# Kernel tuning notes

Measured on AMD Instinct MI355X. Metric: run time of the kernel, lower is better.

## Reference

```python
import jax, jax.numpy as jnp
import numpy as np

B, S, D, F, E = 4, 2048, 1024, 4096, 8
LN_EPS = 1e-5


def setup_inputs() -> dict:
    key = jax.random.key(0)
    ks = jax.random.split(key, 6)
    sc = 0.02
    return {
        "x": jax.random.normal(ks[0], (B, S, D), dtype=jnp.float32),
        "Wr": jax.random.normal(ks[1], (D, E), dtype=jnp.float32) * sc,
        "br": jnp.zeros((E,), jnp.float32),
        "ln_g": jnp.ones((D,), jnp.float32),
        "ln_b": jnp.zeros((D,), jnp.float32),
        "W1": jax.random.normal(ks[2], (E, D, F), dtype=jnp.float32) * sc,
        "b1": jnp.zeros((E, F), jnp.float32),
        "W2": jax.random.normal(ks[3], (E, F, D), dtype=jnp.float32) * sc,
        "b2": jnp.zeros((E, D), jnp.float32),
    }


def reference(x, Wr, br, ln_g, ln_b, W1, b1, W2, b2):
    tokens_shape = x.shape[:-1]
    xt = x.reshape(-1, x.shape[-1])  # [T, D]

    # top-1 routing (eval mode: no jitter noise, no dropout)
    router_logits = xt @ Wr + br                      # [T, E]
    router_probs = jax.nn.softmax(router_logits, axis=-1)
    gates = jnp.max(router_probs, axis=-1, keepdims=True)   # [T, 1]
    idx = jnp.argmax(router_probs, axis=-1)                 # [T] int
    onehot = jax.nn.one_hot(idx, E, dtype=xt.dtype)         # [T, E]

    # layernorm
    mu = jnp.mean(xt, axis=-1, keepdims=True)
    var = jnp.mean(jnp.square(xt - mu), axis=-1, keepdims=True)
    xn = (xt - mu) * jax.lax.rsqrt(var + LN_EPS) * ln_g + ln_b

    # expert FFN: per-token expert-specific GEMMs expressed via one-hot dispatch
    h = jnp.einsum('te,td,edf->tf', onehot, xn, W1) + b1[idx]  # [T, F]
    h = jax.nn.relu(h)
    y = jnp.einsum('te,tf,efd->td', onehot, h, W2) + b2[idx]   # [T, D]

    y = y * gates
    return y.reshape(tokens_shape + (y.shape[-1],))
```

## Files before the change

kernel.cpp:

```cpp
#include <hip/hip_runtime.h>
#include <stdint.h>

#define T_TOK 8192
#define DDIM  1024
#define FDIM  4096
#define NEXP  8
#define BM 128
#define BK 64
#define MAX_MT (T_TOK / BM + NEXP)

typedef __attribute__((ext_vector_type(8))) short bf16x8;
typedef __attribute__((ext_vector_type(8))) unsigned short u16x8;
typedef __attribute__((ext_vector_type(4))) float f32x4;

__device__ __forceinline__ unsigned short f2bf(float f) {
    union { float f; unsigned u; } v; v.f = f;
    unsigned u = v.u;
    u += 0x7fffu + ((u >> 16) & 1u);
    return (unsigned short)(u >> 16);
}

__device__ __forceinline__ void async16(const void* g, void* l) {
    __builtin_amdgcn_global_load_lds(
        (const __attribute__((address_space(1))) unsigned int*)g,
        (__attribute__((address_space(3))) unsigned int*)l, 16, 0, 0);
}

__global__ __launch_bounds__(256) void init_kernel(
    const float* __restrict__ Wr, float* __restrict__ WrT, int* __restrict__ meta) {
    int idx = blockIdx.x * 256 + threadIdx.x;
    if (idx < 16) meta[idx] = 0;
    float v = Wr[idx];
    WrT[(idx & 7) * DDIM + (idx >> 3)] = v;
}

__global__ __launch_bounds__(256) void prep(
    const float* __restrict__ x, const float* __restrict__ WrT, const float* __restrict__ br,
    const float* __restrict__ lng, const float* __restrict__ lnb,
    const float* __restrict__ W1, const float* __restrict__ W2,
    unsigned short* __restrict__ xn, unsigned short* __restrict__ W1t,
    unsigned short* __restrict__ W2t, float* __restrict__ gate,
    int* __restrict__ expert, int* __restrict__ counts) {
    __shared__ float smem[64 * 65];
    int b = blockIdx.x, tid = threadIdx.x;
    int r3 = b % 3, q = b / 3;

    if (r3 != 0) {
        const float* src; unsigned short* dst; int R, C, e, c0, r0;
        if (r3 == 1) {
            R = DDIM; C = FDIM;
            e = q >> 10;
            c0 = (q & 63) * 64; r0 = ((q >> 6) & 15) * 64;
            src = W1; dst = W1t;
        } else {
            R = FDIM; C = DDIM;
            e = q >> 10;
            c0 = (q & 15) * 64; r0 = ((q >> 4) & 63) * 64;
            src = W2; dst = W2t;
        }
        const float* s = src + (size_t)e * R * C;
        unsigned short* d = dst + (size_t)e * R * C;
        float (*tile)[65] = (float(*)[65])smem;
        int lr = tid >> 4, lc = (tid & 15) * 4;
#pragma unroll
        for (int i = 0; i < 4; i++) {
            float4 v = *(const float4*)&s[(size_t)(r0 + lr + i * 16) * C + c0 + lc];
            tile[lr + i * 16][lc + 0] = v.x;
            tile[lr + i * 16][lc + 1] = v.y;
            tile[lr + i * 16][lc + 2] = v.z;
            tile[lr + i * 16][lc + 3] = v.w;
        }
        __syncthreads();
#pragma unroll
        for (int i = 0; i < 2; i++) {
            int ix = tid + i * 256;
            int drow = ix >> 3, seg = ix & 7;
            u16x8 o;
#pragma unroll
            for (int j = 0; j < 8; j++) o[j] = f2bf(tile[seg * 8 + j][drow]);
            *(u16x8*)&d[(size_t)(c0 + drow) * R + r0 + seg * 8] = o;
        }
        return;
    }

    int t = q;
    const float* xrow = x + (size_t)t * DDIM;
    float4 xv = ((const float4*)xrow)[tid];
    float s  = xv.x + xv.y + xv.z + xv.w;
    float sq = xv.x * xv.x + xv.y * xv.y + xv.z * xv.z + xv.w * xv.w;
    ((float2*)smem)[tid] = make_float2(s, sq);

    int e = tid >> 5, l32 = tid & 31;
    const float* wrow = WrT + e * DDIM + l32;
    const float* xp = xrow + l32;
    float a0 = 0, a1 = 0, a2 = 0, a3 = 0;
#pragma unroll
    for (int j = 0; j < 32; j += 4) {
        a0 += xp[32 * j]       * wrow[32 * j];
        a1 += xp[32 * (j + 1)] * wrow[32 * (j + 1)];
        a2 += xp[32 * (j + 2)] * wrow[32 * (j + 2)];
        a3 += xp[32 * (j + 3)] * wrow[32 * (j + 3)];
    }
    float acc = (a0 + a1) + (a2 + a3);
#pragma unroll
    for (int o = 16; o > 0; o >>= 1) acc += __shfl_down(acc, o, 32);
    if ((tid & 31) == 0) smem[512 + e] = acc;
    __syncthreads();

    if (tid < 64) {
        float2 p0 = ((float2*)smem)[tid];
        float2 p1 = ((float2*)smem)[tid + 64];
        float2 p2 = ((float2*)smem)[tid + 128];
        float2 p3 = ((float2*)smem)[tid + 192];
        float ss = (p0.x + p1.x) + (p2.x + p3.x);
        float qq = (p0.y + p1.y) + (p2.y + p3.y);
#pragma unroll
        for (int o = 32; o > 0; o >>= 1) {
            ss += __shfl_down(ss, o);
            qq += __shfl_down(qq, o);
        }
        if (tid == 0) {
            float mu = ss * (1.f / DDIM);
            float var = qq * (1.f / DDIM) - mu * mu;
            float rstd = rsqrtf(var + 1e-5f);
            int best = 0; float bl = -3.4e38f;
            float L[8];
            for (int k = 0; k < 8; k++) {
                float l = smem[512 + k] + br[k];
                L[k] = l;
                if (l > bl) { bl = l; best = k; }
            }
            float den = 0;
            for (int k = 0; k < 8; k++) den += __expf(L[k] - bl);
            gate[t] = 1.f / den;
            expert[t] = best;
            atomicAdd(&counts[best], 1);
            smem[520] = mu; smem[521] = rstd;
        }
    }
    __syncthreads();
    float mu = smem[520], rstd = smem[521];
    float4 gg = ((const float4*)lng)[tid];
    float4 bb = ((const float4*)lnb)[tid];
    ushort4 o;
    o.x = f2bf((xv.x - mu) * rstd * gg.x + bb.x);
    o.y = f2bf((xv.y - mu) * rstd * gg.y + bb.y);
    o.z = f2bf((xv.z - mu) * rstd * gg.z + bb.z);
    o.w = f2bf((xv.w - mu) * rstd * gg.w + bb.w);
    *(ushort4*)(xn + (size_t)t * DDIM + tid * 4) = o;
}

__global__ __launch_bounds__(256) void scatter_perm(
    const int* __restrict__ expert, const int* __restrict__ counts,
    int* __restrict__ fill, int* __restrict__ perm) {
    __shared__ int offs_s[NEXP];
    if (threadIdx.x < NEXP) {
        int o = 0;
        for (int i = 0; i < (int)threadIdx.x; i++) o += counts[i];
        offs_s[threadIdx.x] = o;
    }
    __syncthreads();
    int t = blockIdx.x * 256 + threadIdx.x;
    int e = expert[t];
    int p = atomicAdd(&fill[e], 1);
    perm[offs_s[e] + p] = t;
}

template <int MODE>
__global__ __launch_bounds__(256) void gemm_grouped(
    const unsigned short* __restrict__ A, const unsigned short* __restrict__ Bt,
    const float* __restrict__ bias, unsigned short* __restrict__ Hout,
    float* __restrict__ Yout, const float* __restrict__ gate,
    const int* __restrict__ perm, const int* __restrict__ counts,
    int K, int N) {
    constexpr int BN_   = (MODE == 0) ? 128 : 64;
    constexpr int AI    = (MODE == 0) ? 4 : 2;
    constexpr int BPASS = (MODE == 0) ? 4 : 2;

    int rem = blockIdx.x;
    int e, off = 0, cnt = 0; bool found = false;
    for (e = 0; e < NEXP; e++) {
        cnt = counts[e];
        int mt = (cnt + (BM - 1)) >> 7;
        if (rem < mt) { found = true; break; }
        rem -= mt; off += cnt;
    }
    if (!found) return;
    int mbase = rem << 7;
    int mrem = cnt - mbase;
    int n0 = blockIdx.y * BN_;

    __shared__ __align__(16) unsigned short Alds[BM * BK];
    __shared__ __align__(16) unsigned short Blds[BN_ * BK];

    int tid = threadIdx.x;
    int lane = tid & 63, wave = tid >> 6;
    int grow = lane >> 3;
    int seg  = lane & 7;
    int gseg = seg ^ grow;

    const unsigned short* ag[4];
    unsigned short* al[4];
    const unsigned short* bg[BPASS];
    unsigned short* bl[BPASS];
#pragma unroll
    for (int p = 0; p < 4; p++) {
        int r = p * 32 + wave * 8 + grow;
        int rr = (r < mrem) ? r : 0;
        int t = (MODE == 0) ? perm[off + mbase + rr] : (off + mbase + rr);
        ag[p] = A + (size_t)t * K + gseg * 8;
        al[p] = &Alds[(p * 32 + wave * 8) * BK];
    }
#pragma unroll
    for (int p = 0; p < BPASS; p++) {
        int r = p * 32 + wave * 8 + grow;
        bg[p] = Bt + ((size_t)e * N + n0 + r) * K + gseg * 8;
        bl[p] = &Blds[(p * 32 + wave * 8) * BK];
    }

    int wr = (MODE == 0) ? (wave >> 1) * 64 : wave * 32;
    int wc = (MODE == 0) ? (wave & 1) * 64 : 0;
    int q = lane >> 4, l16 = lane & 15;
    int sx = l16 & 7;

    f32x4 acc[AI][4] = {};

    for (int k0 = 0; k0 < K; k0 += BK) {
#pragma unroll
        for (int p = 0; p < 4; p++) async16(ag[p] + k0, al[p]);
#pragma unroll
        for (int p = 0; p < BPASS; p++) async16(bg[p] + k0, bl[p]);
        __syncthreads();
#pragma unroll
        for (int kk = 0; kk < 2; kk++) {
            int slot = ((kk * 4 + q) ^ sx) * 8;
            bf16x8 af[AI], bfr[4];
#pragma unroll
            for (int i = 0; i < AI; i++)
                af[i] = *(const bf16x8*)&Alds[(wr + i * 16 + l16) * BK + slot];
#pragma unroll
            for (int j = 0; j < 4; j++)
                bfr[j] = *(const bf16x8*)&Blds[(wc + j * 16 + l16) * BK + slot];
#pragma unroll
            for (int i = 0; i < AI; i++)
#pragma unroll
                for (int j = 0; j < 4; j++)
                    acc[i][j] = __builtin_amdgcn_mfma_f32_16x16x32_bf16(af[i], bfr[j], acc[i][j], 0, 0, 0);
        }
        __syncthreads();
    }

    float bs[4];
#pragma unroll
    for (int j = 0; j < 4; j++) bs[j] = bias[(size_t)e * N + n0 + wc + j * 16 + l16];
#pragma unroll
    for (int i = 0; i < AI; i++) {
#pragma unroll
        for (int r = 0; r < 4; r++) {
            int lrow = wr + i * 16 + q * 4 + r;
            if (lrow < mrem) {
                if (MODE == 0) {
                    unsigned short* hp = Hout + (size_t)(off + mbase + lrow) * N + n0 + wc + l16;
#pragma unroll
                    for (int j = 0; j < 4; j++) {
                        float v = acc[i][j][r] + bs[j];
                        hp[j * 16] = f2bf(fmaxf(v, 0.f));
                    }
                } else {
                    int t = perm[off + mbase + lrow];
                    float gt = gate[t];
                    float* yp = Yout + (size_t)t * N + n0 + wc + l16;
#pragma unroll
                    for (int j = 0; j < 4; j++)
                        yp[j * 16] = (acc[i][j][r] + bs[j]) * gt;
                }
            }
        }
    }
}

extern "C" void kernel_launch(void* const* d_in, const int* in_sizes, int n_in,
                              void* d_out, int out_size, void* d_ws, size_t ws_size,
                              hipStream_t stream) {
    const float* x   = (const float*)d_in[0];
    const float* Wr  = (const float*)d_in[1];
    const float* br  = (const float*)d_in[2];
    const float* lng = (const float*)d_in[3];
    const float* lnb = (const float*)d_in[4];
    const float* W1  = (const float*)d_in[5];
    const float* b1  = (const float*)d_in[6];
    const float* W2  = (const float*)d_in[7];
    const float* b2  = (const float*)d_in[8];
    float* out = (float*)d_out;

    char* ws = (char*)d_ws;
    size_t o = 0;
    unsigned short* W1t = (unsigned short*)(ws + o); o += (size_t)NEXP * DDIM * FDIM * 2;
    unsigned short* W2t = (unsigned short*)(ws + o); o += (size_t)NEXP * DDIM * FDIM * 2;
    unsigned short* xn  = (unsigned short*)(ws + o); o += (size_t)T_TOK * DDIM * 2;
    unsigned short* h   = (unsigned short*)(ws + o); o += (size_t)T_TOK * FDIM * 2;
    float* gate = (float*)(ws + o); o += (size_t)T_TOK * 4;
    float* WrT  = (float*)(ws + o); o += (size_t)NEXP * DDIM * 4;
    int* expert = (int*)(ws + o);   o += (size_t)T_TOK * 4;
    int* perm   = (int*)(ws + o);   o += (size_t)T_TOK * 4;
    int* meta   = (int*)(ws + o);
    int* counts = meta;
    int* fill   = meta + 8;

    init_kernel<<<32, 256, 0, stream>>>(Wr, WrT, meta);
    prep<<<3 * T_TOK, 256, 0, stream>>>(x, WrT, br, lng, lnb, W1, W2,
                                        xn, W1t, W2t, gate, expert, counts);
    scatter_perm<<<T_TOK / 256, 256, 0, stream>>>(expert, counts, fill, perm);
    gemm_grouped<0><<<dim3(MAX_MT, FDIM / 128), 256, 0, stream>>>(
        xn, W1t, b1, h, nullptr, nullptr, perm, counts, DDIM, FDIM);
    gemm_grouped<1><<<dim3(MAX_MT, DDIM / 64), 256, 0, stream>>>(
        h, W2t, b2, nullptr, out, gate, perm, counts, FDIM, DDIM);
}
```

Baseline: 618.9 us.

## Use 128x128 tiles with split-K and atomic accumulation in second grouped GEMM

The down-projection GEMM now uses the same 128x128 output tile as the first GEMM, which gives each block more data reuse, and splits K=4096 into two halves so the grid stays about the same size. Partial results are combined with float atomicAdd into the output, so the output is zeroed first by extra blocks added to the prep kernel. The bias is added only by the first K half. In exchange the GEMM pays for atomic traffic, the prep grid grows by a third to zero the output, and the summation order is no longer deterministic.

```diff
diff --git a/kernel.cpp b/kernel.cpp
--- a/kernel.cpp
+++ b/kernel.cpp
@@ -40,14 +40,19 @@
     const float* __restrict__ W1, const float* __restrict__ W2,
     unsigned short* __restrict__ xn, unsigned short* __restrict__ W1t,
     unsigned short* __restrict__ W2t, float* __restrict__ gate,
-    int* __restrict__ expert, int* __restrict__ counts) {
+    int* __restrict__ expert, int* __restrict__ counts, float* __restrict__ y) {
     __shared__ float smem[64 * 65];
     int b = blockIdx.x, tid = threadIdx.x;
-    int r3 = b % 3, q = b / 3;
-
-    if (r3 != 0) {
+    int r4 = b & 3, q = b >> 2;
+
+    if (r4 == 3) {
+        float4 z = make_float4(0.f, 0.f, 0.f, 0.f);
+        ((float4*)y)[(size_t)q * 256 + tid] = z;
+        return;
+    }
+    if (r4 != 0) {
         const float* src; unsigned short* dst; int R, C, e, c0, r0;
-        if (r3 == 1) {
+        if (r4 == 1) {
             R = DDIM; C = FDIM;
             e = q >> 10;
             c0 = (q & 63) * 64; r0 = ((q >> 6) & 15) * 64;
@@ -173,10 +178,6 @@
     float* __restrict__ Yout, const float* __restrict__ gate,
     const int* __restrict__ perm, const int* __restrict__ counts,
     int K, int N) {
-    constexpr int BN_   = (MODE == 0) ? 128 : 64;
-    constexpr int AI    = (MODE == 0) ? 4 : 2;
-    constexpr int BPASS = (MODE == 0) ? 4 : 2;
-
     int rem = blockIdx.x;
     int e, off = 0, cnt = 0; bool found = false;
     for (e = 0; e < NEXP; e++) {
@@ -188,10 +189,17 @@
     if (!found) return;
     int mbase = rem << 7;
     int mrem = cnt - mbase;
-    int n0 = blockIdx.y * BN_;
+    int n0, kbase, kend, kh;
+    if (MODE == 0) {
+        n0 = blockIdx.y << 7; kbase = 0; kend = K; kh = 0;
+    } else {
+        n0 = (blockIdx.y >> 1) << 7;
+        kh = blockIdx.y & 1;
+        kbase = kh * (K >> 1); kend = kbase + (K >> 1);
+    }
 
     __shared__ __align__(16) unsigned short Alds[BM * BK];
-    __shared__ __align__(16) unsigned short Blds[BN_ * BK];
+    __shared__ __align__(16) unsigned short Blds[128 * BK];
 
     int tid = threadIdx.x;
     int lane = tid & 63, wave = tid >> 6;
@@ -201,8 +209,8 @@
 
     const unsigned short* ag[4];
     unsigned short* al[4];
-    const unsigned short* bg[BPASS];
-    unsigned short* bl[BPASS];
+    const unsigned short* bg[4];
+    unsigned short* bl[4];
 #pragma unroll
     for (int p = 0; p < 4; p++) {
         int r = p * 32 + wave * 8 + grow;
@@ -210,39 +218,34 @@
         int t = (MODE == 0) ? perm[off + mbase + rr] : (off + mbase + rr);
         ag[p] = A + (size_t)t * K + gseg * 8;
         al[p] = &Alds[(p * 32 + wave * 8) * BK];
-    }
-#pragma unroll
-    for (int p = 0; p < BPASS; p++) {
-        int r = p * 32 + wave * 8 + grow;
         bg[p] = Bt + ((size_t)e * N + n0 + r) * K + gseg * 8;
         bl[p] = &Blds[(p * 32 + wave * 8) * BK];
     }
 
-    int wr = (MODE == 0) ? (wave >> 1) * 64 : wave * 32;
-    int wc = (MODE == 0) ? (wave & 1) * 64 : 0;
+    int wr = (wave >> 1) * 64, wc = (wave & 1) * 64;
     int q = lane >> 4, l16 = lane & 15;
     int sx = l16 & 7;
 
-    f32x4 acc[AI][4] = {};
-
-    for (int k0 = 0; k0 < K; k0 += BK) {
+    f32x4 acc[4][4] = {};
+
+    for (int k0 = kbase; k0 < kend; k0 += BK) {
 #pragma unroll
         for (int p = 0; p < 4; p++) async16(ag[p] + k0, al[p]);
 #pragma unroll
-        for (int p = 0; p < BPASS; p++) async16(bg[p] + k0, bl[p]);
+        for (int p = 0; p < 4; p++) async16(bg[p] + k0, bl[p]);
         __syncthreads();
 #pragma unroll
         for (int kk = 0; kk < 2; kk++) {
             int slot = ((kk * 4 + q) ^ sx) * 8;
-            bf16x8 af[AI], bfr[4];
-#pragma unroll
-            for (int i = 0; i < AI; i++)
+            bf16x8 af[4], bfr[4];
+#pragma unroll
+            for (int i = 0; i < 4; i++)
                 af[i] = *(const bf16x8*)&Alds[(wr + i * 16 + l16) * BK + slot];
 #pragma unroll
             for (int j = 0; j < 4; j++)
                 bfr[j] = *(const bf16x8*)&Blds[(wc + j * 16 + l16) * BK + slot];
 #pragma unroll
-            for (int i = 0; i < AI; i++)
+            for (int i = 0; i < 4; i++)
 #pragma unroll
                 for (int j = 0; j < 4; j++)
                     acc[i][j] = __builtin_amdgcn_mfma_f32_16x16x32_bf16(af[i], bfr[j], acc[i][j], 0, 0, 0);
@@ -254,7 +257,7 @@
 #pragma unroll
     for (int j = 0; j < 4; j++) bs[j] = bias[(size_t)e * N + n0 + wc + j * 16 + l16];
 #pragma unroll
-    for (int i = 0; i < AI; i++) {
+    for (int i = 0; i < 4; i++) {
 #pragma unroll
         for (int r = 0; r < 4; r++) {
             int lrow = wr + i * 16 + q * 4 + r;
@@ -271,8 +274,10 @@
                     float gt = gate[t];
                     float* yp = Yout + (size_t)t * N + n0 + wc + l16;
 #pragma unroll
-                    for (int j = 0; j < 4; j++)
-                        yp[j * 16] = (acc[i][j][r] + bs[j]) * gt;
+                    for (int j = 0; j < 4; j++) {
+                        float v = (acc[i][j][r] + (kh ? 0.f : bs[j])) * gt;
+                        atomicAdd(&yp[j * 16], v);
+                    }
                 }
             }
         }
@@ -308,11 +313,11 @@
     int* fill   = meta + 8;
 
     init_kernel<<<32, 256, 0, stream>>>(Wr, WrT, meta);
-    prep<<<3 * T_TOK, 256, 0, stream>>>(x, WrT, br, lng, lnb, W1, W2,
-                                        xn, W1t, W2t, gate, expert, counts);
+    prep<<<4 * T_TOK, 256, 0, stream>>>(x, WrT, br, lng, lnb, W1, W2,
+                                        xn, W1t, W2t, gate, expert, counts, out);
     scatter_perm<<<T_TOK / 256, 256, 0, stream>>>(expert, counts, fill, perm);
     gemm_grouped<0><<<dim3(MAX_MT, FDIM / 128), 256, 0, stream>>>(
         xn, W1t, b1, h, nullptr, nullptr, perm, counts, DDIM, FDIM);
-    gemm_grouped<1><<<dim3(MAX_MT, DDIM / 64), 256, 0, stream>>>(
+    gemm_grouped<1><<<dim3(MAX_MT, (DDIM / 128) * 2), 256, 0, stream>>>(
         h, W2t, b2, nullptr, out, gate, perm, counts, FDIM, DDIM);
 }
```

Measured after the change: 666.9 us. 1.08x slower.
